# Kernel optimization log

Measured on AMD Instinct MI355X. Metric: run time of the kernel, lower is better.

Reference implementation:

```python
import jax, jax.numpy as jnp
import numpy as np
from jax import lax

B, L, H = 4096, 2048, 256


def setup_inputs() -> dict:
    key = jax.random.key(0)
    ks = jax.random.split(key, 7)
    s = 1.0 / np.sqrt(H)
    u = lambda k, shape: jax.random.uniform(k, shape, jnp.float32, -s, s)
    return {
        "x": jax.random.normal(ks[0], (B, L), jnp.float32),
        "W_ih": u(ks[1], (H, 1)),
        "b_ih": u(ks[2], (H,)),
        "W_hh": u(ks[3], (H, H)),
        "b_hh": u(ks[4], (H,)),
        "W_lin": u(ks[5], (1, H)),
        "b_lin": u(ks[6], (1,)),
        "future": 128,
    }


def reference(x, W_ih, b_ih, W_hh, b_hh, W_lin, b_lin, future):
    # RNNCell: h' = tanh(x_t W_ih^T + b_ih + h W_hh^T + b_hh); x_t is [B,1]
    def cell(inp, h):
        return jnp.tanh(inp @ W_ih.T + b_ih + h @ W_hh.T + b_hh)

    def lin(h):  # [B,H] -> [B]
        return (h @ W_lin.T + b_lin)[:, 0]

    def step(h, x_t):  # x_t: [B]
        h = cell(x_t[:, None], h)
        return h, lin(h)

    h0 = jnp.zeros((x.shape[0], W_hh.shape[0]), x.dtype)
    h, outs = lax.scan(step, h0, x.T)  # outs: [L, B]

    def fstep(carry, _):
        h, o = carry
        h = cell(o[:, None], h)
        o2 = lin(h)
        return (h, o2), o2

    (_, _), fouts = lax.scan(fstep, (h, outs[-1]), None, length=future)  # [future, B]
    return jnp.concatenate([outs, fouts], axis=0).T  # [B, L+future]
```

## Files before the change

kernel.cpp:

```cpp
#include <hip/hip_runtime.h>
#include <hip/hip_bf16.h>

typedef _Float16 half8 __attribute__((ext_vector_type(8)));
typedef _Float16 half4 __attribute__((ext_vector_type(4)));
typedef float    floatx4 __attribute__((ext_vector_type(4)));

#define B_TOT 4096
#define L_SEQ 2048
#define H_DIM 256
#define FUT   128
#define T_TOT (L_SEQ + FUT)
#define ROWS  16
#define CHUNK 128

__device__ __forceinline__ float tanh_fast(float p) {
    float e = __builtin_amdgcn_exp2f(p * 2.885390082f);
    return __builtin_fmaf(-2.0f, __builtin_amdgcn_rcpf(e + 1.0f), 1.0f);
}

__global__ __launch_bounds__(512, 2) void rnn_seq_kernel(
    const float* __restrict__ x,
    const float* __restrict__ W_ih,
    const float* __restrict__ b_ih,
    const float* __restrict__ W_hh,
    const float* __restrict__ b_hh,
    const float* __restrict__ W_lin,
    const float* __restrict__ b_lin,
    float* __restrict__ out)
{
    __shared__ __align__(16) unsigned char hbuf[2][ROWS * H_DIM * 2];
    __shared__ __align__(16) float xbuf[CHUNK * 17];
    __shared__ __align__(16) float obuf2[2][32][17];

    const int tid  = threadIdx.x;
    const int l    = tid & 63;
    const int w    = tid >> 6;
    const int ln15 = l & 15;
    const int lg   = l >> 4;
    const int b0   = blockIdx.x * ROWS;

    half8 wf[2][8];
    #pragma unroll
    for (int i = 0; i < 2; ++i) {
        const int n = (2 * w + i) * 16 + ln15;
        #pragma unroll
        for (int kk = 0; kk < 8; ++kk) {
            const float* p = W_hh + n * H_DIM + kk * 32 + lg * 8;
            half8 v;
            #pragma unroll
            for (int j = 0; j < 8; ++j) v[j] = (_Float16)p[j];
            wf[i][kk] = v;
        }
    }
    half8 wlf[8];
    #pragma unroll
    for (int kk = 0; kk < 8; ++kk) {
        const int kbase = kk * 32 + lg * 8;
        half8 v;
        #pragma unroll
        for (int j = 0; j < 8; ++j)
            v[j] = ((ln15 & 3) == 0) ? (_Float16)W_lin[kbase + j] : (_Float16)0.0f;
        wlf[kk] = v;
    }
    floatx4 wih4[2], bia4[2];
    #pragma unroll
    for (int i = 0; i < 2; ++i) {
        const int n0 = (2 * w + i) * 16 + lg * 4;
        #pragma unroll
        for (int r = 0; r < 4; ++r) {
            wih4[i][r] = W_ih[n0 + r];
            bia4[i][r] = b_ih[n0 + r] + b_hh[n0 + r];
        }
    }
    const float blin = b_lin[0];

    int aoff[8];
    #pragma unroll
    for (int kk = 0; kk < 8; ++kk)
        aoff[kk] = (ln15 * 512 + kk * 64 + lg * 16) ^ ((ln15 & 7) << 4);
    int woff2[2];
    #pragma unroll
    for (int i = 0; i < 2; ++i)
        woff2[i] = (ln15 * 512 + (2 * w + i) * 32 + lg * 8) ^ ((ln15 & 7) << 4);

    *(floatx4*)(hbuf[0] + tid * 16) = floatx4{0.f, 0.f, 0.f, 0.f};
    __syncthreads();

    int cur = 0;

    for (int s = 1; s <= L_SEQ; ++s) {
        const int t_out = s - 2;

        if (t_out >= 34 && (t_out & 31) == 2) {
            const int tb = t_out - 34, par = (tb >> 5) & 1;
            const int rr = tid >> 5, tt = tid & 31;
            out[(size_t)(b0 + rr) * T_TOT + tb + tt] = obuf2[par][tt][rr] + blin;
        }
        if (((s - 1) & (CHUNK - 1)) == 0) {
            #pragma unroll
            for (int jj = 0; jj < 4; ++jj) {
                const int idx = jj * 512 + tid;
                const int rr = idx >> 7, tl = idx & 127;
                xbuf[tl * 17 + rr] = x[(size_t)(b0 + rr) * L_SEQ + (s - 1) + tl];
            }
            __syncthreads();
        }

        half8 a[8];
        #pragma unroll
        for (int kk = 0; kk < 8; ++kk)
            a[kk] = *(const half8*)(hbuf[cur] + aoff[kk]);
        const float xm = xbuf[((s - 1) & (CHUNK - 1)) * 17 + ln15];

        floatx4 acc[2][2];
        #pragma unroll
        for (int i = 0; i < 2; ++i) {
            #pragma unroll
            for (int r = 0; r < 4; ++r)
                acc[i][0][r] = __builtin_fmaf(xm, wih4[i][r], bia4[i][r]);
            acc[i][1] = floatx4{0, 0, 0, 0};
        }
        #pragma unroll
        for (int kk = 0; kk < 8; ++kk) {
            acc[0][kk & 1] = __builtin_amdgcn_mfma_f32_16x16x32_f16(wf[0][kk], a[kk], acc[0][kk & 1], 0, 0, 0);
            acc[1][kk & 1] = __builtin_amdgcn_mfma_f32_16x16x32_f16(wf[1][kk], a[kk], acc[1][kk & 1], 0, 0, 0);
        }
        #pragma unroll
        for (int i = 0; i < 2; ++i) {
            const floatx4 av = acc[i][0] + acc[i][1];
            half4 hv;
            #pragma unroll
            for (int r = 0; r < 4; ++r) hv[r] = (_Float16)tanh_fast(av[r]);
            *(half4*)(hbuf[cur ^ 1] + woff2[i]) = hv;
        }
        __syncthreads();

        if (w == 0 && s >= 2) {
            floatx4 al0 = floatx4{0,0,0,0}, al1 = floatx4{0,0,0,0};
            #pragma unroll
            for (int kk = 0; kk < 8; ++kk) {
                if (kk & 1) al1 = __builtin_amdgcn_mfma_f32_16x16x32_f16(wlf[kk], a[kk], al1, 0, 0, 0);
                else        al0 = __builtin_amdgcn_mfma_f32_16x16x32_f16(wlf[kk], a[kk], al0, 0, 0, 0);
            }
            if (lg == 0)
                obuf2[(t_out >> 5) & 1][t_out & 31][ln15] = al0[0] + al1[0];
        }
        cur ^= 1;
    }

    for (int s = L_SEQ + 1; s <= T_TOT; ++s) {
        const int t_out = s - 2;
        if ((t_out & 31) == 2) {
            const int tb = t_out - 34, par = (tb >> 5) & 1;
            const int rr = tid >> 5, tt = tid & 31;
            out[(size_t)(b0 + rr) * T_TOT + tb + tt] = obuf2[par][tt][rr] + blin;
        }
        half8 a[8];
        #pragma unroll
        for (int kk = 0; kk < 8; ++kk)
            a[kk] = *(const half8*)(hbuf[cur] + aoff[kk]);

        floatx4 al0 = floatx4{0,0,0,0}, al1 = floatx4{0,0,0,0};
        #pragma unroll
        for (int kk = 0; kk < 8; ++kk) {
            if (kk & 1) al1 = __builtin_amdgcn_mfma_f32_16x16x32_f16(wlf[kk], a[kk], al1, 0, 0, 0);
            else        al0 = __builtin_amdgcn_mfma_f32_16x16x32_f16(wlf[kk], a[kk], al0, 0, 0, 0);
        }
        floatx4 acc[2][2];
        #pragma unroll
        for (int i = 0; i < 2; ++i) {
            acc[i][0] = bia4[i];
            acc[i][1] = floatx4{0, 0, 0, 0};
        }
        #pragma unroll
        for (int kk = 0; kk < 8; ++kk) {
            acc[0][kk & 1] = __builtin_amdgcn_mfma_f32_16x16x32_f16(wf[0][kk], a[kk], acc[0][kk & 1], 0, 0, 0);
            acc[1][kk & 1] = __builtin_amdgcn_mfma_f32_16x16x32_f16(wf[1][kk], a[kk], acc[1][kk & 1], 0, 0, 0);
        }
        if (w == 0 && lg == 0)
            obuf2[(t_out >> 5) & 1][t_out & 31][ln15] = al0[0] + al1[0];

        const float xm = al0[0] + al1[0] + blin;
        #pragma unroll
        for (int i = 0; i < 2; ++i) {
            const floatx4 av = acc[i][0] + acc[i][1];
            half4 hv;
            #pragma unroll
            for (int r = 0; r < 4; ++r)
                hv[r] = (_Float16)tanh_fast(__builtin_fmaf(xm, wih4[i][r], av[r]));
            *(half4*)(hbuf[cur ^ 1] + woff2[i]) = hv;
        }
        __syncthreads();
        cur ^= 1;
    }

    if (w == 0) {
        half8 a[8];
        #pragma unroll
        for (int kk = 0; kk < 8; ++kk)
            a[kk] = *(const half8*)(hbuf[cur] + aoff[kk]);
        floatx4 al0 = floatx4{0,0,0,0}, al1 = floatx4{0,0,0,0};
        #pragma unroll
        for (int kk = 0; kk < 8; ++kk) {
            if (kk & 1) al1 = __builtin_amdgcn_mfma_f32_16x16x32_f16(wlf[kk], a[kk], al1, 0, 0, 0);
            else        al0 = __builtin_amdgcn_mfma_f32_16x16x32_f16(wlf[kk], a[kk], al0, 0, 0, 0);
        }
        if (lg == 0) obuf2[1][31][ln15] = al0[0] + al1[0];
    }
    __syncthreads();
    {
        const int rr = tid >> 5, tt = tid & 31;
        out[(size_t)(b0 + rr) * T_TOT + 2144 + tt] = obuf2[1][tt][rr] + blin;
    }
}

extern "C" void kernel_launch(void* const* d_in, const int* in_sizes, int n_in,
                              void* d_out, int out_size, void* d_ws, size_t ws_size,
                              hipStream_t stream) {
    const float* x     = (const float*)d_in[0];
    const float* W_ih  = (const float*)d_in[1];
    const float* b_ih  = (const float*)d_in[2];
    const float* W_hh  = (const float*)d_in[3];
    const float* b_hh  = (const float*)d_in[4];
    const float* W_lin = (const float*)d_in[5];
    const float* b_lin = (const float*)d_in[6];
    float* out = (float*)d_out;
    rnn_seq_kernel<<<B_TOT / ROWS, 512, 0, stream>>>(x, W_ih, b_ih, W_hh, b_hh, W_lin, b_lin, out);
}
```

Baseline: 1.574 ms.

## Replace per-step barriers with LDS flag spin-waits and triple-buffered hidden state

```diff
diff --git a/kernel.cpp b/kernel.cpp
--- a/kernel.cpp
+++ b/kernel.cpp
@@ -11,7 +11,6 @@
 #define FUT   128
 #define T_TOT (L_SEQ + FUT)
 #define ROWS  16
-#define CHUNK 128
 
 __device__ __forceinline__ float tanh_fast(float p) {
     float e = __builtin_amdgcn_exp2f(p * 2.885390082f);
@@ -28,9 +27,9 @@
     const float* __restrict__ b_lin,
     float* __restrict__ out)
 {
-    __shared__ __align__(16) unsigned char hbuf[2][ROWS * H_DIM * 2];
-    __shared__ __align__(16) float xbuf[CHUNK * 17];
-    __shared__ __align__(16) float obuf2[2][32][17];
+    __shared__ __align__(16) unsigned char hbuf[3][ROWS * 512];
+    __shared__ __align__(16) float obuf[64][17];
+    __shared__ int flags[8];
 
     const int tid  = threadIdx.x;
     const int l    = tid & 63;
@@ -38,6 +37,7 @@
     const int ln15 = l & 15;
     const int lg   = l >> 4;
     const int b0   = blockIdx.x * ROWS;
+    volatile int* vflags = flags;
 
     half8 wf[2][8];
     #pragma unroll
@@ -52,17 +52,8 @@
             wf[i][kk] = v;
         }
     }
-    half8 wlf[8];
-    #pragma unroll
-    for (int kk = 0; kk < 8; ++kk) {
-        const int kbase = kk * 32 + lg * 8;
-        half8 v;
-        #pragma unroll
-        for (int j = 0; j < 8; ++j)
-            v[j] = ((ln15 & 3) == 0) ? (_Float16)W_lin[kbase + j] : (_Float16)0.0f;
-        wlf[kk] = v;
-    }
     floatx4 wih4[2], bia4[2];
+    float wlp[2][4];
     #pragma unroll
     for (int i = 0; i < 2; ++i) {
         const int n0 = (2 * w + i) * 16 + lg * 4;
@@ -70,6 +61,7 @@
         for (int r = 0; r < 4; ++r) {
             wih4[i][r] = W_ih[n0 + r];
             bia4[i][r] = b_ih[n0 + r] + b_hh[n0 + r];
+            wlp[i][r]  = W_lin[n0 + r];
         }
     }
     const float blin = b_lin[0];
@@ -84,33 +76,50 @@
         woff2[i] = (ln15 * 512 + (2 * w + i) * 32 + lg * 8) ^ ((ln15 & 7) << 4);
 
     *(floatx4*)(hbuf[0] + tid * 16) = floatx4{0.f, 0.f, 0.f, 0.f};
+    #pragma unroll
+    for (int i = 0; i < 3; ++i) {
+        const int idx = i * 512 + tid;
+        if (idx < 64 * 17) ((float*)obuf)[idx] = 0.f;
+    }
+    if (tid < 8) flags[tid] = 0;
     __syncthreads();
 
-    int cur = 0;
+    float xm = x[(size_t)(b0 + ln15) * L_SEQ + 0];
+    int rb = 0, wb = 1;
+
+#define SPIN_WAIT(tgt)                                                        \
+    do {                                                                      \
+        int m_;                                                               \
+        do {                                                                  \
+            int f0 = vflags[0], f1 = vflags[1], f2 = vflags[2], f3 = vflags[3]; \
+            int f4 = vflags[4], f5 = vflags[5], f6 = vflags[6], f7 = vflags[7]; \
+            int a_ = f0 < f1 ? f0 : f1;  int b_ = f2 < f3 ? f2 : f3;          \
+            int c_ = f4 < f5 ? f4 : f5;  int d_ = f6 < f7 ? f6 : f7;          \
+            int e_ = a_ < b_ ? a_ : b_;  int g_ = c_ < d_ ? c_ : d_;          \
+            m_ = e_ < g_ ? e_ : g_;                                           \
+        } while (m_ < (tgt));                                                 \
+        asm volatile("" ::: "memory");                                        \
+    } while (0)
+
+#define FLUSH_RING()                                                          \
+    do {                                                                      \
+        const int tb = s - 35;                                                \
+        const int rr = tid >> 5, tt = tid & 31;                               \
+        const int slot = (tb + tt) & 63;                                      \
+        const float v_ = obuf[slot][rr];                                      \
+        out[(size_t)(b0 + rr) * T_TOT + tb + tt] = v_ + blin;                 \
+        obuf[slot][rr] = 0.f;                                                 \
+    } while (0)
 
     for (int s = 1; s <= L_SEQ; ++s) {
-        const int t_out = s - 2;
-
-        if (t_out >= 34 && (t_out & 31) == 2) {
-            const int tb = t_out - 34, par = (tb >> 5) & 1;
-            const int rr = tid >> 5, tt = tid & 31;
-            out[(size_t)(b0 + rr) * T_TOT + tb + tt] = obuf2[par][tt][rr] + blin;
-        }
-        if (((s - 1) & (CHUNK - 1)) == 0) {
-            #pragma unroll
-            for (int jj = 0; jj < 4; ++jj) {
-                const int idx = jj * 512 + tid;
-                const int rr = idx >> 7, tl = idx & 127;
-                xbuf[tl * 17 + rr] = x[(size_t)(b0 + rr) * L_SEQ + (s - 1) + tl];
-            }
-            __syncthreads();
-        }
-
+        SPIN_WAIT(s - 1);
+        const unsigned char* hb = hbuf[rb];
         half8 a[8];
         #pragma unroll
         for (int kk = 0; kk < 8; ++kk)
-            a[kk] = *(const half8*)(hbuf[cur] + aoff[kk]);
-        const float xm = xbuf[((s - 1) & (CHUNK - 1)) * 17 + ln15];
+            a[kk] = *(const half8*)(hb + aoff[kk]);
+        float xnext = 0.0f;
+        if (s < L_SEQ) xnext = x[(size_t)(b0 + ln15) * L_SEQ + s];
 
         floatx4 acc[2][2];
         #pragma unroll
@@ -125,51 +134,52 @@
             acc[0][kk & 1] = __builtin_amdgcn_mfma_f32_16x16x32_f16(wf[0][kk], a[kk], acc[0][kk & 1], 0, 0, 0);
             acc[1][kk & 1] = __builtin_amdgcn_mfma_f32_16x16x32_f16(wf[1][kk], a[kk], acc[1][kk & 1], 0, 0, 0);
         }
+        unsigned char* hw = hbuf[wb];
+        float tv[2][4];
         #pragma unroll
         for (int i = 0; i < 2; ++i) {
             const floatx4 av = acc[i][0] + acc[i][1];
             half4 hv;
             #pragma unroll
-            for (int r = 0; r < 4; ++r) hv[r] = (_Float16)tanh_fast(av[r]);
-            *(half4*)(hbuf[cur ^ 1] + woff2[i]) = hv;
-        }
-        __syncthreads();
-
-        if (w == 0 && s >= 2) {
-            floatx4 al0 = floatx4{0,0,0,0}, al1 = floatx4{0,0,0,0};
-            #pragma unroll
-            for (int kk = 0; kk < 8; ++kk) {
-                if (kk & 1) al1 = __builtin_amdgcn_mfma_f32_16x16x32_f16(wlf[kk], a[kk], al1, 0, 0, 0);
-                else        al0 = __builtin_amdgcn_mfma_f32_16x16x32_f16(wlf[kk], a[kk], al0, 0, 0, 0);
+            for (int r = 0; r < 4; ++r) {
+                tv[i][r] = tanh_fast(av[r]);
+                hv[r] = (_Float16)tv[i][r];
             }
-            if (lg == 0)
-                obuf2[(t_out >> 5) & 1][t_out & 31][ln15] = al0[0] + al1[0];
-        }
-        cur ^= 1;
+            *(half4*)(hw + woff2[i]) = hv;
+        }
+        float part = 0.f;
+        #pragma unroll
+        for (int i = 0; i < 2; ++i)
+            #pragma unroll
+            for (int r = 0; r < 4; ++r)
+                part = __builtin_fmaf(tv[i][r], wlp[i][r], part);
+        part += __shfl_xor(part, 16);
+        part += __shfl_xor(part, 32);
+        if (l < 16) atomicAdd(&obuf[(s - 1) & 63][l], part);
+
+        asm volatile("s_waitcnt lgkmcnt(0)" ::: "memory");
+        if (l == 0) vflags[w] = s;
+
+        if (s >= 35 && (s & 31) == 3) FLUSH_RING();
+        xm = xnext;
+        rb = wb; wb = (wb == 2) ? 0 : wb + 1;
     }
 
     for (int s = L_SEQ + 1; s <= T_TOT; ++s) {
-        const int t_out = s - 2;
-        if ((t_out & 31) == 2) {
-            const int tb = t_out - 34, par = (tb >> 5) & 1;
-            const int rr = tid >> 5, tt = tid & 31;
-            out[(size_t)(b0 + rr) * T_TOT + tb + tt] = obuf2[par][tt][rr] + blin;
-        }
+        SPIN_WAIT(s - 1);
+        const unsigned char* hb = hbuf[rb];
         half8 a[8];
         #pragma unroll
         for (int kk = 0; kk < 8; ++kk)
-            a[kk] = *(const half8*)(hbuf[cur] + aoff[kk]);
-
-        floatx4 al0 = floatx4{0,0,0,0}, al1 = floatx4{0,0,0,0};
-        #pragma unroll
-        for (int kk = 0; kk < 8; ++kk) {
-            if (kk & 1) al1 = __builtin_amdgcn_mfma_f32_16x16x32_f16(wlf[kk], a[kk], al1, 0, 0, 0);
-            else        al0 = __builtin_amdgcn_mfma_f32_16x16x32_f16(wlf[kk], a[kk], al0, 0, 0, 0);
-        }
+            a[kk] = *(const half8*)(hb + aoff[kk]);
+        const float xf = obuf[(s - 2) & 63][ln15] + blin;
+
         floatx4 acc[2][2];
         #pragma unroll
         for (int i = 0; i < 2; ++i) {
-            acc[i][0] = bia4[i];
+            #pragma unroll
+            for (int r = 0; r < 4; ++r)
+                acc[i][0][r] = __builtin_fmaf(xf, wih4[i][r], bia4[i][r]);
             acc[i][1] = floatx4{0, 0, 0, 0};
         }
         #pragma unroll
@@ -177,41 +187,43 @@
             acc[0][kk & 1] = __builtin_amdgcn_mfma_f32_16x16x32_f16(wf[0][kk], a[kk], acc[0][kk & 1], 0, 0, 0);
             acc[1][kk & 1] = __builtin_amdgcn_mfma_f32_16x16x32_f16(wf[1][kk], a[kk], acc[1][kk & 1], 0, 0, 0);
         }
-        if (w == 0 && lg == 0)
-            obuf2[(t_out >> 5) & 1][t_out & 31][ln15] = al0[0] + al1[0];
-
-        const float xm = al0[0] + al1[0] + blin;
+        unsigned char* hw = hbuf[wb];
+        float tv[2][4];
         #pragma unroll
         for (int i = 0; i < 2; ++i) {
             const floatx4 av = acc[i][0] + acc[i][1];
             half4 hv;
             #pragma unroll
-            for (int r = 0; r < 4; ++r)
-                hv[r] = (_Float16)tanh_fast(__builtin_fmaf(xm, wih4[i][r], av[r]));
-            *(half4*)(hbuf[cur ^ 1] + woff2[i]) = hv;
-        }
-        __syncthreads();
-        cur ^= 1;
-    }
-
-    if (w == 0) {
-        half8 a[8];
-        #pragma unroll
-        for (int kk = 0; kk < 8; ++kk)
-            a[kk] = *(const half8*)(hbuf[cur] + aoff[kk]);
-        floatx4 al0 = floatx4{0,0,0,0}, al1 = floatx4{0,0,0,0};
-        #pragma unroll
-        for (int kk = 0; kk < 8; ++kk) {
-            if (kk & 1) al1 = __builtin_amdgcn_mfma_f32_16x16x32_f16(wlf[kk], a[kk], al1, 0, 0, 0);
-            else        al0 = __builtin_amdgcn_mfma_f32_16x16x32_f16(wlf[kk], a[kk], al0, 0, 0, 0);
-        }
-        if (lg == 0) obuf2[1][31][ln15] = al0[0] + al1[0];
-    }
+            for (int r = 0; r < 4; ++r) {
+                tv[i][r] = tanh_fast(av[r]);
+                hv[r] = (_Float16)tv[i][r];
+            }
+            *(half4*)(hw + woff2[i]) = hv;
+        }
+        float part = 0.f;
+        #pragma unroll
+        for (int i = 0; i < 2; ++i)
+            #pragma unroll
+            for (int r = 0; r < 4; ++r)
+                part = __builtin_fmaf(tv[i][r], wlp[i][r], part);
+        part += __shfl_xor(part, 16);
+        part += __shfl_xor(part, 32);
+        if (l < 16) atomicAdd(&obuf[(s - 1) & 63][l], part);
+
+        asm volatile("s_waitcnt lgkmcnt(0)" ::: "memory");
+        if (l == 0) vflags[w] = s;
+
+        if ((s & 31) == 3) FLUSH_RING();
+        rb = wb; wb = (wb == 2) ? 0 : wb + 1;
+    }
+
     __syncthreads();
     {
         const int rr = tid >> 5, tt = tid & 31;
-        out[(size_t)(b0 + rr) * T_TOT + 2144 + tt] = obuf2[1][tt][rr] + blin;
-    }
+        out[(size_t)(b0 + rr) * T_TOT + 2144 + tt] = obuf[32 + tt][rr] + blin;
+    }
+#undef SPIN_WAIT
+#undef FLUSH_RING
 }
 
 extern "C" void kernel_launch(void* const* d_in, const int* in_sizes, int n_in,
```

After: 2.234 ms. +41.9%, slower.

## Prefetch x per step in registers and split tile MFMA chains to overlap tanh

Applied to the files above, without the earlier changes.

```diff
diff --git a/kernel.cpp b/kernel.cpp
--- a/kernel.cpp
+++ b/kernel.cpp
@@ -11,7 +11,6 @@
 #define FUT   128
 #define T_TOT (L_SEQ + FUT)
 #define ROWS  16
-#define CHUNK 128
 
 __device__ __forceinline__ float tanh_fast(float p) {
     float e = __builtin_amdgcn_exp2f(p * 2.885390082f);
@@ -29,7 +28,6 @@
     float* __restrict__ out)
 {
     __shared__ __align__(16) unsigned char hbuf[2][ROWS * H_DIM * 2];
-    __shared__ __align__(16) float xbuf[CHUNK * 17];
     __shared__ __align__(16) float obuf2[2][32][17];
 
     const int tid  = threadIdx.x;
@@ -87,6 +85,8 @@
     __syncthreads();
 
     int cur = 0;
+    const float* xrow = x + (size_t)(b0 + ln15) * L_SEQ;
+    float xr = xrow[0];
 
     for (int s = 1; s <= L_SEQ; ++s) {
         const int t_out = s - 2;
@@ -96,42 +96,48 @@
             const int rr = tid >> 5, tt = tid & 31;
             out[(size_t)(b0 + rr) * T_TOT + tb + tt] = obuf2[par][tt][rr] + blin;
         }
-        if (((s - 1) & (CHUNK - 1)) == 0) {
-            #pragma unroll
-            for (int jj = 0; jj < 4; ++jj) {
-                const int idx = jj * 512 + tid;
-                const int rr = idx >> 7, tl = idx & 127;
-                xbuf[tl * 17 + rr] = x[(size_t)(b0 + rr) * L_SEQ + (s - 1) + tl];
-            }
-            __syncthreads();
-        }
 
         half8 a[8];
         #pragma unroll
         for (int kk = 0; kk < 8; ++kk)
             a[kk] = *(const half8*)(hbuf[cur] + aoff[kk]);
-        const float xm = xbuf[((s - 1) & (CHUNK - 1)) * 17 + ln15];
-
-        floatx4 acc[2][2];
-        #pragma unroll
-        for (int i = 0; i < 2; ++i) {
-            #pragma unroll
-            for (int r = 0; r < 4; ++r)
-                acc[i][0][r] = __builtin_fmaf(xm, wih4[i][r], bia4[i][r]);
-            acc[i][1] = floatx4{0, 0, 0, 0};
-        }
-        #pragma unroll
-        for (int kk = 0; kk < 8; ++kk) {
-            acc[0][kk & 1] = __builtin_amdgcn_mfma_f32_16x16x32_f16(wf[0][kk], a[kk], acc[0][kk & 1], 0, 0, 0);
-            acc[1][kk & 1] = __builtin_amdgcn_mfma_f32_16x16x32_f16(wf[1][kk], a[kk], acc[1][kk & 1], 0, 0, 0);
-        }
-        #pragma unroll
-        for (int i = 0; i < 2; ++i) {
-            const floatx4 av = acc[i][0] + acc[i][1];
+
+        const float xm = xr;
+        if (s < L_SEQ) xr = xrow[s];
+
+        floatx4 acc00, acc01;
+        #pragma unroll
+        for (int r = 0; r < 4; ++r)
+            acc00[r] = __builtin_fmaf(xm, wih4[0][r], bia4[0][r]);
+        acc01 = floatx4{0, 0, 0, 0};
+        #pragma unroll
+        for (int kk = 0; kk < 8; ++kk) {
+            if (kk & 1) acc01 = __builtin_amdgcn_mfma_f32_16x16x32_f16(wf[0][kk], a[kk], acc01, 0, 0, 0);
+            else        acc00 = __builtin_amdgcn_mfma_f32_16x16x32_f16(wf[0][kk], a[kk], acc00, 0, 0, 0);
+        }
+        {
+            const floatx4 av = acc00 + acc01;
             half4 hv;
             #pragma unroll
             for (int r = 0; r < 4; ++r) hv[r] = (_Float16)tanh_fast(av[r]);
-            *(half4*)(hbuf[cur ^ 1] + woff2[i]) = hv;
+            *(half4*)(hbuf[cur ^ 1] + woff2[0]) = hv;
+        }
+        floatx4 acc10, acc11;
+        #pragma unroll
+        for (int r = 0; r < 4; ++r)
+            acc10[r] = __builtin_fmaf(xm, wih4[1][r], bia4[1][r]);
+        acc11 = floatx4{0, 0, 0, 0};
+        #pragma unroll
+        for (int kk = 0; kk < 8; ++kk) {
+            if (kk & 1) acc11 = __builtin_amdgcn_mfma_f32_16x16x32_f16(wf[1][kk], a[kk], acc11, 0, 0, 0);
+            else        acc10 = __builtin_amdgcn_mfma_f32_16x16x32_f16(wf[1][kk], a[kk], acc10, 0, 0, 0);
+        }
+        {
+            const floatx4 av = acc10 + acc11;
+            half4 hv;
+            #pragma unroll
+            for (int r = 0; r < 4; ++r) hv[r] = (_Float16)tanh_fast(av[r]);
+            *(half4*)(hbuf[cur ^ 1] + woff2[1]) = hv;
         }
         __syncthreads();
 
@@ -161,11 +167,6 @@
             a[kk] = *(const half8*)(hbuf[cur] + aoff[kk]);
 
         floatx4 al0 = floatx4{0,0,0,0}, al1 = floatx4{0,0,0,0};
-        #pragma unroll
-        for (int kk = 0; kk < 8; ++kk) {
-            if (kk & 1) al1 = __builtin_amdgcn_mfma_f32_16x16x32_f16(wlf[kk], a[kk], al1, 0, 0, 0);
-            else        al0 = __builtin_amdgcn_mfma_f32_16x16x32_f16(wlf[kk], a[kk], al0, 0, 0, 0);
-        }
         floatx4 acc[2][2];
         #pragma unroll
         for (int i = 0; i < 2; ++i) {
@@ -174,6 +175,8 @@
         }
         #pragma unroll
         for (int kk = 0; kk < 8; ++kk) {
+            if (kk & 1) al1 = __builtin_amdgcn_mfma_f32_16x16x32_f16(wlf[kk], a[kk], al1, 0, 0, 0);
+            else        al0 = __builtin_amdgcn_mfma_f32_16x16x32_f16(wlf[kk], a[kk], al0, 0, 0, 0);
             acc[0][kk & 1] = __builtin_amdgcn_mfma_f32_16x16x32_f16(wf[0][kk], a[kk], acc[0][kk & 1], 0, 0, 0);
             acc[1][kk & 1] = __builtin_amdgcn_mfma_f32_16x16x32_f16(wf[1][kk], a[kk], acc[1][kk & 1], 0, 0, 0);
         }
```

Result: no change. 1.596 ms (+1.4%).
